# Performance work log

Hardware: AMD Instinct MI355X
Metric: run time of the kernel (lower is better)

The kernel has to match this reference:

```python
import jax, jax.numpy as jnp
import numpy as np

B, S, D = 2, 2048, 1024
H, L = 16, 512
DH = D // H
LN_EPS = 1e-5


def setup_inputs() -> dict:
    key = jax.random.key(0)
    ks = jax.random.split(key, 6)
    w = 0.02  # init scale for weights
    return {
        "x": jax.random.normal(ks[0], (B, S, D), jnp.float32),
        "W_q": jax.random.normal(ks[1], (D, D), jnp.float32) * w,
        "W_dkv": jax.random.normal(ks[2], (L, D), jnp.float32) * w,
        "W_uk": jax.random.normal(ks[3], (D, L), jnp.float32) * w,
        "W_uv": jax.random.normal(ks[4], (D, L), jnp.float32) * w,
        "W_o": jax.random.normal(ks[5], (D, D), jnp.float32) * w,
        "ln_gamma": jnp.ones((L,), jnp.float32),
        "ln_beta": jnp.zeros((L,), jnp.float32),
    }


def reference(x, W_q, W_dkv, W_uk, W_uv, W_o, ln_gamma, ln_beta):
    # latent KV: LayerNorm(x @ W_dkv^T)  -> [B, S, L]
    c = x @ W_dkv.T
    mu = jnp.mean(c, axis=-1, keepdims=True)
    var = jnp.mean((c - mu) ** 2, axis=-1, keepdims=True)
    c_kv = (c - mu) * jax.lax.rsqrt(var + LN_EPS) * ln_gamma + ln_beta

    # absorbed key projection: (W_q @ W_uk) viewed per head  -> [H, DH, L]
    absorbed_k = (W_q @ W_uk).reshape(H, DH, L)

    # q is raw x reshaped per head (W_q absorbed)  -> [B, S, H, DH]
    q = x.reshape(B, S, H, DH)
    tmp = jnp.einsum('bshd,hdl->bhsl', q, absorbed_k)         # [B,H,S,L]
    scores = jnp.einsum('bhsl,btl->bhst', tmp, c_kv) / np.sqrt(DH)

    # causal mask (past_length = 0, no kv_cache -> S_full == S)
    mask = jnp.tril(jnp.ones((S, S), bool))
    scores = jnp.where(mask[None, None], scores, -1e30)
    attn = jax.nn.softmax(scores, axis=-1)                    # [B,H,S,S]

    # values decompressed from latent  -> [B, S, H, DH]
    v = (c_kv @ W_uv.T).reshape(B, S, H, DH)
    ctx = jnp.einsum('bhst,bthd->bshd', attn, v).reshape(B, S, D)
    out = ctx @ W_o.T
    return out, c_kv
```

## Files before the change

### kernel.cpp

```cpp
#include <hip/hip_runtime.h>


typedef __attribute__((ext_vector_type(4))) float f32x4;
typedef __attribute__((ext_vector_type(8))) unsigned short u16x8;
typedef __attribute__((ext_vector_type(4))) unsigned short u16x4;
typedef __attribute__((ext_vector_type(8))) __bf16 bf16x8;

__device__ __forceinline__ unsigned short f2bf(float f) {
  unsigned int u = __builtin_bit_cast(unsigned int, f);
  u += 0x7FFFu + ((u >> 16) & 1u);
  return (unsigned short)(u >> 16);
}
__device__ __forceinline__ unsigned short f2bf_rz(float f) {
  return (unsigned short)(__builtin_bit_cast(unsigned int, f) >> 16);
}
__device__ __forceinline__ float bf2f(unsigned short u) {
  return __builtin_bit_cast(float, (unsigned int)u << 16);
}

__device__ __forceinline__ f32x4 mfma16(u16x8 a, u16x8 b, f32x4 c) {
  return __builtin_amdgcn_mfma_f32_16x16x32_bf16(
      __builtin_bit_cast(bf16x8, a), __builtin_bit_cast(bf16x8, b), c, 0, 0, 0);
}

__device__ __forceinline__ void gload_lds16(const void* g, void* l) {
  __builtin_amdgcn_global_load_lds(
      (const __attribute__((address_space(1))) unsigned int*)g,
      (__attribute__((address_space(3))) unsigned int*)l, 16, 0, 0);
}

__global__ __launch_bounds__(256)
void fused_cvt(const float* __restrict__ x, unsigned short* __restrict__ xb,
               const float* __restrict__ wq, unsigned short* __restrict__ wqb,
               const float* __restrict__ wdkv, unsigned short* __restrict__ wdkvb,
               const float* __restrict__ wuv, unsigned short* __restrict__ wuvb,
               const float* __restrict__ wo, unsigned short* __restrict__ wob,
               const float* __restrict__ wuk, unsigned short* __restrict__ wukT) {
  __shared__ float t[64][65];
  if (blockIdx.x >= 2048) {
    int bid = blockIdx.x - 2048;
    int c0 = (bid & 7) * 64;
    int r0 = (bid >> 3) * 64;
    int lr = threadIdx.x >> 4, lc = (threadIdx.x & 15) * 4;
#pragma unroll
    for (int i = 0; i < 4; i++) {
      int row = lr + i * 16;
      float4 v = *(const float4*)(wuk + (size_t)(r0 + row) * 512 + c0 + lc);
      t[row][lc] = v.x; t[row][lc + 1] = v.y; t[row][lc + 2] = v.z; t[row][lc + 3] = v.w;
    }
    __syncthreads();
#pragma unroll
    for (int i = 0; i < 4; i++) {
      int oc = lr + i * 16;
      u16x4 o;
      o[0] = f2bf(t[lc + 0][oc]); o[1] = f2bf(t[lc + 1][oc]);
      o[2] = f2bf(t[lc + 2][oc]); o[3] = f2bf(t[lc + 3][oc]);
      *(u16x4*)(wukT + (size_t)(c0 + oc) * 1024 + r0 + lc) = o;
    }
    return;
  }
  const int total = 1048576 + 262144 + 131072 + 131072 + 262144;
  for (int i = blockIdx.x * 256 + threadIdx.x; i < total; i += 2048 * 256) {
    const float* src; unsigned short* dst; int off;
    if (i < 1048576)      { src = x;    dst = xb;    off = i; }
    else if (i < 1310720) { src = wq;   dst = wqb;   off = i - 1048576; }
    else if (i < 1441792) { src = wdkv; dst = wdkvb; off = i - 1310720; }
    else if (i < 1572864) { src = wuv;  dst = wuvb;  off = i - 1441792; }
    else                  { src = wo;   dst = wob;   off = i - 1572864; }
    float4 v = ((const float4*)src)[off];
    u16x4 o;
    o[0] = f2bf(v.x); o[1] = f2bf(v.y); o[2] = f2bf(v.z); o[3] = f2bf(v.w);
    ((u16x4*)dst)[off] = o;
  }
}

template <int MODE, int IM, int JF, int MINW>
__global__ __launch_bounds__(256, MINW)
void gemm_bt(const unsigned short* __restrict__ A, const unsigned short* __restrict__ B,
             void* __restrict__ C1, void* __restrict__ C2,
             int M, int N, int K, int lda, int ldb, int ldc) {
  constexpr int BM = IM * 32, BN = JF * 32;
  __shared__ __align__(16) unsigned short sA[2][BM * 64];
  __shared__ __align__(16) unsigned short sB[2][BN * 64];
  const int tid = threadIdx.x;
  const int w = tid >> 6, ln = tid & 63;
  const int m0 = blockIdx.y * BM, n0 = blockIdx.x * BN;
  const int wm = (w >> 1) * (IM * 16), wn = (w & 1) * (JF * 16);
  const int c16 = ln & 15, g = ln >> 4;
  f32x4 zero = {0.f, 0.f, 0.f, 0.f};
  f32x4 acc[IM][JF];
#pragma unroll
  for (int i = 0; i < IM; i++)
#pragma unroll
    for (int j = 0; j < JF; j++) acc[i][j] = zero;

#define STAGE_G(kt, bf)                                                        \
  {                                                                            \
    _Pragma("unroll") for (int l = 0; l < BM / 32; l++) {                      \
      int c = l * 256 + tid;                                                   \
      int row = c >> 3, pc = c & 7;                                            \
      gload_lds16(A + (size_t)(m0 + row) * lda + (kt) + ((pc ^ (row & 7)) << 3),\
                  (char*)&sA[bf][0] + (l * 256 + w * 64) * 16);                \
    }                                                                          \
    _Pragma("unroll") for (int l = 0; l < BN / 32; l++) {                      \
      int c = l * 256 + tid;                                                   \
      int row = c >> 3, pc = c & 7;                                            \
      gload_lds16(B + (size_t)(n0 + row) * ldb + (kt) + ((pc ^ (row & 7)) << 3),\
                  (char*)&sB[bf][0] + (l * 256 + w * 64) * 16);                \
    }                                                                          \
  }

  STAGE_G(0, 0);
  __syncthreads();
  int bf = 0;
  for (int kt = 0; kt < K; kt += 64) {
    if (kt + 64 < K) STAGE_G(kt + 64, bf ^ 1);
    u16x8 af[IM][2], bfr[JF][2];
#pragma unroll
    for (int i = 0; i < IM; i++) {
      int ra = wm + i * 16 + c16;
#pragma unroll
      for (int kk = 0; kk < 2; kk++)
        af[i][kk] = *(const u16x8*)((const char*)&sA[bf][0] + ra * 128 +
                                    ((((kk << 2) + g) ^ (ra & 7)) << 4));
    }
#pragma unroll
    for (int j = 0; j < JF; j++) {
      int rb = wn + j * 16 + c16;
#pragma unroll
      for (int kk = 0; kk < 2; kk++)
        bfr[j][kk] = *(const u16x8*)((const char*)&sB[bf][0] + rb * 128 +
                                     ((((kk << 2) + g) ^ (rb & 7)) << 4));
    }
#pragma unroll
    for (int kk = 0; kk < 2; kk++)
#pragma unroll
      for (int i = 0; i < IM; i++)
#pragma unroll
        for (int j = 0; j < JF; j++)
          acc[i][j] = mfma16(af[i][kk], bfr[j][kk], acc[i][j]);
    __syncthreads();
    bf ^= 1;
  }
#undef STAGE_G
  const int row0 = m0 + wm + g * 4;
  const int col0 = n0 + wn + c16;
  if (MODE == 1) {
    float* C = (float*)C1;
#pragma unroll
    for (int i = 0; i < IM; i++)
#pragma unroll
      for (int j = 0; j < JF; j++)
#pragma unroll
        for (int r = 0; r < 4; r++)
          C[(size_t)(row0 + i * 16 + r) * ldc + col0 + j * 16] = acc[i][j][r];
  } else if (MODE == 0) {
    unsigned short* C = (unsigned short*)C1;
#pragma unroll
    for (int i = 0; i < IM; i++)
#pragma unroll
      for (int j = 0; j < JF; j++)
#pragma unroll
        for (int r = 0; r < 4; r++)
          C[(size_t)(row0 + i * 16 + r) * ldc + col0 + j * 16] = f2bf(acc[i][j][r]);
  } else {
    if (n0 < 1024) {
      unsigned short* C = (unsigned short*)C1;
#pragma unroll
      for (int i = 0; i < IM; i++)
#pragma unroll
        for (int j = 0; j < JF; j++)
#pragma unroll
          for (int r = 0; r < 4; r++)
            C[(size_t)(row0 + i * 16 + r) * ldc + col0 + j * 16] = f2bf(acc[i][j][r]);
    } else {
      unsigned short* C = (unsigned short*)C2;
#pragma unroll
      for (int i = 0; i < IM; i++)
#pragma unroll
        for (int j = 0; j < JF; j++) {
          u16x4 t4;
#pragma unroll
          for (int r = 0; r < 4; r++) t4[r] = f2bf(acc[i][j][r]);
          *(u16x4*)(C + (size_t)(col0 + j * 16 - 1024) * 4096 + row0 + i * 16) = t4;
        }
    }
  }
}

__global__ __launch_bounds__(256)
void ln_rows(const float* __restrict__ cin, const float* __restrict__ gamma,
             const float* __restrict__ beta, float* __restrict__ of32,
             unsigned short* __restrict__ obf) {
  int row = blockIdx.x * 4 + (threadIdx.x >> 6);
  int ln = threadIdx.x & 63;
  const float* r = cin + (size_t)row * 512 + ln * 8;
  float4 a = *(const float4*)r;
  float4 b = *(const float4*)(r + 4);
  float xv[8] = {a.x, a.y, a.z, a.w, b.x, b.y, b.z, b.w};
  float s = 0.f, q = 0.f;
#pragma unroll
  for (int j = 0; j < 8; j++) { s += xv[j]; q += xv[j] * xv[j]; }
#pragma unroll
  for (int m = 1; m < 64; m <<= 1) { s += __shfl_xor(s, m); q += __shfl_xor(q, m); }
  float mu = s * (1.f / 512.f);
  float var = q * (1.f / 512.f) - mu * mu;
  float rs = rsqrtf(var + 1e-5f);
  float gm[8], bt[8];
  *(float4*)&gm[0] = *(const float4*)(gamma + ln * 8);
  *(float4*)&gm[4] = *(const float4*)(gamma + ln * 8 + 4);
  *(float4*)&bt[0] = *(const float4*)(beta + ln * 8);
  *(float4*)&bt[4] = *(const float4*)(beta + ln * 8 + 4);
  float o[8];
#pragma unroll
  for (int j = 0; j < 8; j++) o[j] = (xv[j] - mu) * rs * gm[j] + bt[j];
  float4 o0 = {o[0], o[1], o[2], o[3]}, o1 = {o[4], o[5], o[6], o[7]};
  *(float4*)(of32 + (size_t)row * 512 + ln * 8) = o0;
  *(float4*)(of32 + (size_t)row * 512 + ln * 8 + 4) = o1;
  u16x8 ob;
#pragma unroll
  for (int j = 0; j < 8; j++) ob[j] = f2bf(o[j]);
  *(u16x8*)(obf + (size_t)row * 512 + ln * 8) = ob;
}

__global__ __launch_bounds__(256, 4)
void mla_attn6(const unsigned short* __restrict__ kabs,
               const unsigned short* __restrict__ xq,
               const unsigned short* __restrict__ vT,
               unsigned short* __restrict__ Opart,
               float* __restrict__ Lpart) {
  __shared__ __align__(16) unsigned short sK[2][64 * 64];
  __shared__ __align__(16) unsigned short sVT[2][64 * 64];
  __shared__ __align__(16) unsigned short sP[4][16 * 40];
  const int tid = threadIdx.x, w = tid >> 6, ln = tid & 63;
  const int g = ln >> 4, c16 = ln & 15;
  const int bh = blockIdx.y;
  const int b = bh >> 4, h = bh & 15;
  int cid = blockIdx.x, qb, ch;
  if (cid < 8)       { qb = cid;                 ch = 0; }
  else if (cid < 24) { qb = 8 + ((cid - 8) >> 1);  ch = (cid - 8) & 1; }
  else if (cid < 48) { qb = 16 + (cid - 24) / 3;   ch = (cid - 24) % 3; }
  else               { qb = 24 + ((cid - 48) >> 2); ch = (cid - 48) & 3; }
  const int ts = ch * 8;
  const int te = min(ts + 8, qb + 1);
  const int q0 = qb * 64;
  const int qw = q0 + w * 16;
  const size_t rowb = (size_t)b * 2048;

  u16x8 qf[2];
  {
    const unsigned short* qp = xq + (rowb + qw + c16) * 1024 + h * 64 + g * 8;
    qf[0] = *(const u16x8*)(qp);
    qf[1] = *(const u16x8*)(qp + 32);
  }
  f32x4 zero = {0.f, 0.f, 0.f, 0.f};
  f32x4 o[4] = {zero, zero, zero, zero};
  float lsum[4] = {0.f, 0.f, 0.f, 0.f};
  const float SC = 0.18033688011112042f;
  const float M0 = 8.f;
  unsigned short* Pw = &sP[w][0];
  const unsigned short* kb_g = kabs + rowb * 1024 + h * 64;
  const unsigned short* vb_g = vT + (size_t)(h * 64) * 4096 + rowb;

#define STAGE_A(tt, bfi)                                                       \
  {                                                                            \
    int t0s = (tt) * 64;                                                       \
    _Pragma("unroll") for (int l = 0; l < 2; l++) {                            \
      int c = l * 256 + tid;                                                   \
      int row = c >> 3, pc = c & 7;                                            \
      gload_lds16(kb_g + (size_t)(t0s + row) * 1024 + ((pc ^ (row & 7)) << 3), \
                  (char*)&sK[bfi][0] + (l * 256 + w * 64) * 16);               \
    }                                                                          \
    _Pragma("unroll") for (int l = 0; l < 2; l++) {                            \
      int c = l * 256 + tid;                                                   \
      int row = c >> 3, pc = c & 7;                                            \
      gload_lds16(vb_g + (size_t)row * 4096 + t0s + ((pc ^ (row & 7)) << 3),   \
                  (char*)&sVT[bfi][0] + (l * 256 + w * 64) * 16);              \
    }                                                                          \
  }

  STAGE_A(ts, 0);
  __syncthreads();
  int bf = 0;
  for (int tt = ts; tt < te; tt++) {
    const int t0 = tt * 64;
    if (tt + 1 < te) STAGE_A(tt + 1, bf ^ 1);
    f32x4 s[4];
#pragma unroll
    for (int nt = 0; nt < 4; nt++) {
      int t = nt * 16 + c16;
      int sw = t & 7;
      const char* kb = (const char*)&sK[bf][0] + t * 128;
      f32x4 a = zero;
      a = mfma16(qf[0], *(const u16x8*)(kb + ((g ^ sw) << 4)), a);
      a = mfma16(qf[1], *(const u16x8*)(kb + (((4 + g) ^ sw) << 4)), a);
      s[nt] = a;
    }
    if (t0 + 63 <= qw) {
#pragma unroll
      for (int nt = 0; nt < 4; nt++)
#pragma unroll
        for (int r = 0; r < 4; r++) {
          float p = exp2f(s[nt][r] * SC - M0);
          lsum[r] += p;
          s[nt][r] = p;
        }
    } else {
#pragma unroll
      for (int nt = 0; nt < 4; nt++) {
        int tcol = t0 + nt * 16 + c16;
#pragma unroll
        for (int r = 0; r < 4; r++) {
          float p = (tcol <= qw + g * 4 + r) ? exp2f(s[nt][r] * SC - M0) : 0.f;
          lsum[r] += p;
          s[nt][r] = p;
        }
      }
    }
#pragma unroll
    for (int half = 0; half < 2; half++) {
#pragma unroll
      for (int ntl = 0; ntl < 2; ntl++)
#pragma unroll
        for (int r = 0; r < 4; r++)
          Pw[(g * 4 + r) * 40 + ntl * 16 + c16] = f2bf_rz(s[half * 2 + ntl][r]);
      u16x8 pa = *(const u16x8*)((const char*)Pw + c16 * 80 + g * 16);
#pragma unroll
      for (int dt = 0; dt < 4; dt++) {
        int d = dt * 16 + c16;
        const char* vb = (const char*)&sVT[bf][0] + d * 128 +
                         ((((half << 2) + g) ^ (d & 7)) << 4);
        o[dt] = mfma16(pa, *(const u16x8*)vb, o[dt]);
      }
    }
    __syncthreads();
    bf ^= 1;
  }
#undef STAGE_A
  unsigned short* op = Opart + ((size_t)bh * 80 + cid) * 4096;
  float* lp = Lpart + ((size_t)bh * 80 + cid) * 64;
#pragma unroll
  for (int r = 0; r < 4; r++) {
    float t = lsum[r];
    t += __shfl_xor(t, 1); t += __shfl_xor(t, 2);
    t += __shfl_xor(t, 4); t += __shfl_xor(t, 8);
    int ql = w * 16 + g * 4 + r;
    if (c16 == 0) lp[ql] = t;
#pragma unroll
    for (int dt = 0; dt < 4; dt++)
      op[ql * 64 + dt * 16 + c16] = f2bf(o[dt][r]);
  }
}

__global__ __launch_bounds__(256)
void attn_combine(const unsigned short* __restrict__ Opart,
                  const float* __restrict__ Lpart,
                  unsigned short* __restrict__ ctx) {
  const int qb = blockIdx.x, bh = blockIdx.y;
  const int b = bh >> 4, h = bh & 15;
  const int ncq = (qb >> 3) + 1;
  const int g8 = qb >> 3;
  const int start = (g8 == 0 ? 0 : (g8 == 1 ? 8 : (g8 == 2 ? 24 : 48)));
  const int cid0 = start + (qb & 7) * ncq;
  const int q = threadIdx.x >> 2;
  const int d0 = (threadIdx.x & 3) * 16;
  float acc[16];
#pragma unroll
  for (int j = 0; j < 16; j++) acc[j] = 0.f;
  float lacc = 0.f;
  for (int c = 0; c < ncq; c++) {
    size_t base = (size_t)bh * 80 + cid0 + c;
    lacc += Lpart[base * 64 + q];
    const unsigned short* op = Opart + base * 4096 + q * 64 + d0;
    u16x8 v0 = *(const u16x8*)(op);
    u16x8 v1 = *(const u16x8*)(op + 8);
#pragma unroll
    for (int j = 0; j < 8; j++) { acc[j] += bf2f(v0[j]); acc[8 + j] += bf2f(v1[j]); }
  }
  float inv = 1.f / lacc;
  u16x8 o0, o1;
#pragma unroll
  for (int j = 0; j < 8; j++) { o0[j] = f2bf(acc[j] * inv); o1[j] = f2bf(acc[8 + j] * inv); }
  unsigned short* cp = ctx + ((size_t)b * 2048 + qb * 64 + q) * 1024 + h * 64 + d0;
  *(u16x8*)(cp) = o0;
  *(u16x8*)(cp + 8) = o1;
}

extern "C" void kernel_launch(void* const* d_in, const int* in_sizes, int n_in,
                              void* d_out, int out_size, void* d_ws, size_t ws_size,
                              hipStream_t stream) {
  const float* x    = (const float*)d_in[0];
  const float* Wq   = (const float*)d_in[1];
  const float* Wdkv = (const float*)d_in[2];
  const float* Wuk  = (const float*)d_in[3];
  const float* Wuv  = (const float*)d_in[4];
  const float* Wo   = (const float*)d_in[5];
  const float* gam  = (const float*)d_in[6];
  const float* bet  = (const float*)d_in[7];
  float* out_f = (float*)d_out;
  float* ckv_f = out_f + (size_t)4096 * 1024;

  char* ws = (char*)d_ws;
  unsigned short* xb     = (unsigned short*)(ws);
  unsigned short* wq_b   = (unsigned short*)(ws + 8388608);
  unsigned short* wdkv_b = (unsigned short*)(ws + 10485760);
  unsigned short* wukT_b = (unsigned short*)(ws + 11534336);
  unsigned short* akt_b  = (unsigned short*)(ws + 12582912);
  unsigned short* wuv_b  = (unsigned short*)(ws + 13631488);
  unsigned short* wo_b   = (unsigned short*)(ws + 14680064);
  unsigned short* ckv_b  = (unsigned short*)(ws + 16777216);
  float*          c_f    = (float*)(ws + 20971520);
  unsigned short* kabs   = (unsigned short*)(ws + 29360128);
  unsigned short* vT     = (unsigned short*)(ws + 37748736);
  unsigned short* ctx_b  = (unsigned short*)(ws + 46137344);
  unsigned short* Opart  = (unsigned short*)(ws + 54525952);
  float*          Lpart  = (float*)(ws + 75497472);

  fused_cvt<<<2176, 256, 0, stream>>>(x, xb, Wq, wq_b, Wdkv, wdkv_b,
                                      Wuv, wuv_b, Wo, wo_b, Wuk, wukT_b);

  gemm_bt<1, 2, 2, 4><<<dim3(8, 64), 256, 0, stream>>>(xb, wdkv_b, c_f, nullptr,
                                                       4096, 512, 1024, 1024, 1024, 512);
  ln_rows<<<1024, 256, 0, stream>>>(c_f, gam, bet, ckv_f, ckv_b);
  gemm_bt<0, 1, 2, 4><<<dim3(8, 32), 256, 0, stream>>>(wq_b, wukT_b, akt_b, nullptr,
                                                       1024, 512, 1024, 1024, 1024, 512);
  gemm_bt<3, 4, 4, 2><<<dim3(16, 32), 256, 0, stream>>>(ckv_b, akt_b, kabs, vT,
                                                        4096, 2048, 512, 512, 512, 1024);
  mla_attn6<<<dim3(80, 32), 256, 0, stream>>>(kabs, xb, vT, Opart, Lpart);
  attn_combine<<<dim3(32, 32), 256, 0, stream>>>(Opart, Lpart, ctx_b);
  gemm_bt<1, 2, 4, 3><<<dim3(8, 64), 256, 0, stream>>>(ctx_b, wo_b, out_f, nullptr,
                                                       4096, 1024, 1024, 1024, 1024, 1024);
}
```

Before: 199.0 us.

## Merge LN with absorbed-key GEMM and fold attention combine into last block

The LayerNorm rows kernel and the small W_q·W_uk GEMM now run in one launch, with extra blocks dispatched to a shared device-side GEMM routine. The split-K attention combine is folded into the attention kernel: each chunk block bumps an atomic counter, and the last block for a query tile reduces the partials and writes ctx. This removes two kernel launches and the gaps between them, at the cost of atomics, thread fences and a counter buffer that fused_cvt must zero on every call.

```diff
diff --git a/kernel.cpp b/kernel.cpp
--- a/kernel.cpp
+++ b/kernel.cpp
@@ -35,8 +35,12 @@
                const float* __restrict__ wdkv, unsigned short* __restrict__ wdkvb,
                const float* __restrict__ wuv, unsigned short* __restrict__ wuvb,
                const float* __restrict__ wo, unsigned short* __restrict__ wob,
-               const float* __restrict__ wuk, unsigned short* __restrict__ wukT) {
+               const float* __restrict__ wuk, unsigned short* __restrict__ wukT,
+               int* __restrict__ cnt) {
   __shared__ float t[64][65];
+  if (blockIdx.x < 4) {
+    cnt[blockIdx.x * 256 + threadIdx.x] = 0;
+  }
   if (blockIdx.x >= 2048) {
     int bid = blockIdx.x - 2048;
     int c0 = (bid & 7) * 64;
@@ -74,17 +78,17 @@
   }
 }
 
-template <int MODE, int IM, int JF, int MINW>
-__global__ __launch_bounds__(256, MINW)
-void gemm_bt(const unsigned short* __restrict__ A, const unsigned short* __restrict__ B,
-             void* __restrict__ C1, void* __restrict__ C2,
-             int M, int N, int K, int lda, int ldb, int ldc) {
+template <int MODE, int IM, int JF>
+__device__ __forceinline__
+void gemm_dev(int bx, int by,
+              const unsigned short* __restrict__ A, const unsigned short* __restrict__ B,
+              void* __restrict__ C1, void* __restrict__ C2,
+              int K, int lda, int ldb, int ldc,
+              unsigned short* sA, unsigned short* sB) {
   constexpr int BM = IM * 32, BN = JF * 32;
-  __shared__ __align__(16) unsigned short sA[2][BM * 64];
-  __shared__ __align__(16) unsigned short sB[2][BN * 64];
   const int tid = threadIdx.x;
   const int w = tid >> 6, ln = tid & 63;
-  const int m0 = blockIdx.y * BM, n0 = blockIdx.x * BN;
+  const int m0 = by * BM, n0 = bx * BN;
   const int wm = (w >> 1) * (IM * 16), wn = (w & 1) * (JF * 16);
   const int c16 = ln & 15, g = ln >> 4;
   f32x4 zero = {0.f, 0.f, 0.f, 0.f};
@@ -94,20 +98,20 @@
 #pragma unroll
     for (int j = 0; j < JF; j++) acc[i][j] = zero;
 
-#define STAGE_G(kt, bf)                                                        \
-  {                                                                            \
-    _Pragma("unroll") for (int l = 0; l < BM / 32; l++) {                      \
-      int c = l * 256 + tid;                                                   \
-      int row = c >> 3, pc = c & 7;                                            \
+#define STAGE_G(kt, bf)                                                         \
+  {                                                                             \
+    _Pragma("unroll") for (int l = 0; l < BM / 32; l++) {                       \
+      int c = l * 256 + tid;                                                    \
+      int row = c >> 3, pc = c & 7;                                             \
       gload_lds16(A + (size_t)(m0 + row) * lda + (kt) + ((pc ^ (row & 7)) << 3),\
-                  (char*)&sA[bf][0] + (l * 256 + w * 64) * 16);                \
-    }                                                                          \
-    _Pragma("unroll") for (int l = 0; l < BN / 32; l++) {                      \
-      int c = l * 256 + tid;                                                   \
-      int row = c >> 3, pc = c & 7;                                            \
+                  (char*)(sA + (bf) * (BM * 64)) + (l * 256 + w * 64) * 16);    \
+    }                                                                           \
+    _Pragma("unroll") for (int l = 0; l < BN / 32; l++) {                       \
+      int c = l * 256 + tid;                                                    \
+      int row = c >> 3, pc = c & 7;                                             \
       gload_lds16(B + (size_t)(n0 + row) * ldb + (kt) + ((pc ^ (row & 7)) << 3),\
-                  (char*)&sB[bf][0] + (l * 256 + w * 64) * 16);                \
-    }                                                                          \
+                  (char*)(sB + (bf) * (BN * 64)) + (l * 256 + w * 64) * 16);    \
+    }                                                                           \
   }
 
   STAGE_G(0, 0);
@@ -121,7 +125,7 @@
       int ra = wm + i * 16 + c16;
 #pragma unroll
       for (int kk = 0; kk < 2; kk++)
-        af[i][kk] = *(const u16x8*)((const char*)&sA[bf][0] + ra * 128 +
+        af[i][kk] = *(const u16x8*)((const char*)(sA + bf * (BM * 64)) + ra * 128 +
                                     ((((kk << 2) + g) ^ (ra & 7)) << 4));
     }
 #pragma unroll
@@ -129,7 +133,7 @@
       int rb = wn + j * 16 + c16;
 #pragma unroll
       for (int kk = 0; kk < 2; kk++)
-        bfr[j][kk] = *(const u16x8*)((const char*)&sB[bf][0] + rb * 128 +
+        bfr[j][kk] = *(const u16x8*)((const char*)(sB + bf * (BN * 64)) + rb * 128 +
                                      ((((kk << 2) + g) ^ (rb & 7)) << 4));
     }
 #pragma unroll
@@ -188,10 +192,31 @@
   }
 }
 
-__global__ __launch_bounds__(256)
-void ln_rows(const float* __restrict__ cin, const float* __restrict__ gamma,
-             const float* __restrict__ beta, float* __restrict__ of32,
-             unsigned short* __restrict__ obf) {
+template <int MODE, int IM, int JF, int MINW>
+__global__ __launch_bounds__(256, MINW)
+void gemm_bt(const unsigned short* __restrict__ A, const unsigned short* __restrict__ B,
+             void* __restrict__ C1, void* __restrict__ C2,
+             int K, int lda, int ldb, int ldc) {
+  __shared__ __align__(16) unsigned short sA[2 * IM * 32 * 64];
+  __shared__ __align__(16) unsigned short sB[2 * JF * 32 * 64];
+  gemm_dev<MODE, IM, JF>(blockIdx.x, blockIdx.y, A, B, C1, C2, K, lda, ldb, ldc,
+                         sA, sB);
+}
+
+__global__ __launch_bounds__(256, 4)
+void lnak(const float* __restrict__ cin, const float* __restrict__ gamma,
+          const float* __restrict__ beta, float* __restrict__ of32,
+          unsigned short* __restrict__ obf,
+          const unsigned short* __restrict__ wqb,
+          const unsigned short* __restrict__ wukT,
+          unsigned short* __restrict__ akt) {
+  __shared__ __align__(16) unsigned short sh[2 * 32 * 64 + 2 * 64 * 64];
+  if (blockIdx.x >= 1024) {
+    int b2 = blockIdx.x - 1024;
+    gemm_dev<0, 1, 2>(b2 & 7, b2 >> 3, wqb, wukT, akt, nullptr,
+                      1024, 1024, 1024, 512, sh, sh + 2 * 32 * 64);
+    return;
+  }
   int row = blockIdx.x * 4 + (threadIdx.x >> 6);
   int ln = threadIdx.x & 63;
   const float* r = cin + (size_t)row * 512 + ln * 8;
@@ -224,14 +249,17 @@
 }
 
 __global__ __launch_bounds__(256, 4)
-void mla_attn6(const unsigned short* __restrict__ kabs,
+void mla_attn7(const unsigned short* __restrict__ kabs,
                const unsigned short* __restrict__ xq,
                const unsigned short* __restrict__ vT,
                unsigned short* __restrict__ Opart,
-               float* __restrict__ Lpart) {
+               float* __restrict__ Lpart,
+               int* __restrict__ cnt,
+               unsigned short* __restrict__ ctx) {
   __shared__ __align__(16) unsigned short sK[2][64 * 64];
   __shared__ __align__(16) unsigned short sVT[2][64 * 64];
   __shared__ __align__(16) unsigned short sP[4][16 * 40];
+  __shared__ int sLast;
   const int tid = threadIdx.x, w = tid >> 6, ln = tid & 63;
   const int g = ln >> 4, c16 = ln & 15;
   const int bh = blockIdx.y;
@@ -241,6 +269,7 @@
   else if (cid < 24) { qb = 8 + ((cid - 8) >> 1);  ch = (cid - 8) & 1; }
   else if (cid < 48) { qb = 16 + (cid - 24) / 3;   ch = (cid - 24) % 3; }
   else               { qb = 24 + ((cid - 48) >> 2); ch = (cid - 48) & 3; }
+  const int ncq = (qb >> 3) + 1;
   const int ts = ch * 8;
   const int te = min(ts + 8, qb + 1);
   const int q0 = qb * 64;
@@ -350,20 +379,18 @@
     for (int dt = 0; dt < 4; dt++)
       op[ql * 64 + dt * 16 + c16] = f2bf(o[dt][r]);
   }
-}
-
-__global__ __launch_bounds__(256)
-void attn_combine(const unsigned short* __restrict__ Opart,
-                  const float* __restrict__ Lpart,
-                  unsigned short* __restrict__ ctx) {
-  const int qb = blockIdx.x, bh = blockIdx.y;
-  const int b = bh >> 4, h = bh & 15;
-  const int ncq = (qb >> 3) + 1;
-  const int g8 = qb >> 3;
-  const int start = (g8 == 0 ? 0 : (g8 == 1 ? 8 : (g8 == 2 ? 24 : 48)));
-  const int cid0 = start + (qb & 7) * ncq;
-  const int q = threadIdx.x >> 2;
-  const int d0 = (threadIdx.x & 3) * 16;
+  __threadfence();
+  __syncthreads();
+  if (tid == 0) {
+    int old = atomicAdd(&cnt[bh * 32 + qb], 1);
+    sLast = (old == ncq - 1);
+  }
+  __syncthreads();
+  if (!sLast) return;
+  __threadfence();
+  const int cid0 = cid - ch;
+  const int q = tid >> 2;
+  const int d0 = (tid & 3) * 16;
   float acc[16];
 #pragma unroll
   for (int j = 0; j < 16; j++) acc[j] = 0.f;
@@ -371,16 +398,19 @@
   for (int c = 0; c < ncq; c++) {
     size_t base = (size_t)bh * 80 + cid0 + c;
     lacc += Lpart[base * 64 + q];
-    const unsigned short* op = Opart + base * 4096 + q * 64 + d0;
-    u16x8 v0 = *(const u16x8*)(op);
-    u16x8 v1 = *(const u16x8*)(op + 8);
+    const unsigned short* op2 = Opart + base * 4096 + q * 64 + d0;
+    u16x8 v0 = *(const u16x8*)(op2);
+    u16x8 v1 = *(const u16x8*)(op2 + 8);
 #pragma unroll
     for (int j = 0; j < 8; j++) { acc[j] += bf2f(v0[j]); acc[8 + j] += bf2f(v1[j]); }
   }
   float inv = 1.f / lacc;
   u16x8 o0, o1;
 #pragma unroll
-  for (int j = 0; j < 8; j++) { o0[j] = f2bf(acc[j] * inv); o1[j] = f2bf(acc[8 + j] * inv); }
+  for (int j = 0; j < 8; j++) {
+    o0[j] = f2bf(acc[j] * inv);
+    o1[j] = f2bf(acc[8 + j] * inv);
+  }
   unsigned short* cp = ctx + ((size_t)b * 2048 + qb * 64 + q) * 1024 + h * 64 + d0;
   *(u16x8*)(cp) = o0;
   *(u16x8*)(cp + 8) = o1;
@@ -415,19 +445,16 @@
   unsigned short* ctx_b  = (unsigned short*)(ws + 46137344);
   unsigned short* Opart  = (unsigned short*)(ws + 54525952);
   float*          Lpart  = (float*)(ws + 75497472);
+  int*            cnt    = (int*)(ws + 76152832);
 
   fused_cvt<<<2176, 256, 0, stream>>>(x, xb, Wq, wq_b, Wdkv, wdkv_b,
-                                      Wuv, wuv_b, Wo, wo_b, Wuk, wukT_b);
-
+                                      Wuv, wuv_b, Wo, wo_b, Wuk, wukT_b, cnt);
   gemm_bt<1, 2, 2, 4><<<dim3(8, 64), 256, 0, stream>>>(xb, wdkv_b, c_f, nullptr,
-                                                       4096, 512, 1024, 1024, 1024, 512);
-  ln_rows<<<1024, 256, 0, stream>>>(c_f, gam, bet, ckv_f, ckv_b);
-  gemm_bt<0, 1, 2, 4><<<dim3(8, 32), 256, 0, stream>>>(wq_b, wukT_b, akt_b, nullptr,
-                                                       1024, 512, 1024, 1024, 1024, 512);
+                                                       1024, 1024, 1024, 512);
+  lnak<<<1280, 256, 0, stream>>>(c_f, gam, bet, ckv_f, ckv_b, wq_b, wukT_b, akt_b);
   gemm_bt<3, 4, 4, 2><<<dim3(16, 32), 256, 0, stream>>>(ckv_b, akt_b, kabs, vT,
-                                                        4096, 2048, 512, 512, 512, 1024);
-  mla_attn6<<<dim3(80, 32), 256, 0, stream>>>(kabs, xb, vT, Opart, Lpart);
-  attn_combine<<<dim3(32, 32), 256, 0, stream>>>(Opart, Lpart, ctx_b);
+                                                        512, 512, 512, 1024);
+  mla_attn7<<<dim3(80, 32), 256, 0, stream>>>(kabs, xb, vT, Opart, Lpart, cnt, ctx_b);
   gemm_bt<1, 2, 4, 3><<<dim3(8, 64), 256, 0, stream>>>(ctx_b, wo_b, out_f, nullptr,
-                                                       4096, 1024, 1024, 1024, 1024, 1024);
-}
+                                                       1024, 1024, 1024, 1024);
+}
```

Result: slower. 704.0 us (+253.7%).
